# Optimization experiments

Measured on AMD Instinct MI355X. Metric: run time of the kernel, lower is better.

## Reference

```python
import jax, jax.numpy as jnp
import numpy as np

D_MODEL = 1024
HEAD_SIZE = 64
BLOCK_SIZE = 2048
B, T = 4, 2048


def setup_inputs() -> dict:
    key = jax.random.key(0)
    ks = jax.random.split(key, 7)
    s = 1.0 / np.sqrt(D_MODEL)
    x = jax.random.normal(ks[0], (B, T, D_MODEL), dtype=jnp.float32)
    Wq = jax.random.uniform(ks[1], (D_MODEL, HEAD_SIZE), jnp.float32, -s, s)
    bq = jax.random.uniform(ks[2], (HEAD_SIZE,), jnp.float32, -s, s)
    Wk = jax.random.uniform(ks[3], (D_MODEL, HEAD_SIZE), jnp.float32, -s, s)
    bk = jax.random.uniform(ks[4], (HEAD_SIZE,), jnp.float32, -s, s)
    Wv = jax.random.uniform(ks[5], (D_MODEL, HEAD_SIZE), jnp.float32, -s, s)
    return {"x": x, "Wq": Wq, "bq": bq, "Wk": Wk, "bk": bk, "Wv": Wv, "mask": 1}


def reference(x, Wq, bq, Wk, bk, Wv, mask):
    # x: [B, T, C]; single attention head, dropout is identity (eval/p=0)
    Tlen = x.shape[1]
    q = x @ Wq + bq              # [B, T, hs]
    k = x @ Wk + bk              # [B, T, hs]
    v = x @ Wv                   # [B, T, hs] (no bias)
    hs = k.shape[-1]
    # Faithful to source: weights = QK^T / hs**(-0.5)  ==  QK^T * sqrt(hs)
    w = jnp.einsum('btd,bsd->bts', q, k) * jnp.sqrt(jnp.asarray(hs, x.dtype))
    if mask:
        causal = jnp.tril(jnp.ones((Tlen, Tlen), dtype=bool))
        w = jnp.where(causal, w, jnp.asarray(-jnp.inf, w.dtype))
    w = jax.nn.softmax(w, axis=-1)
    out = jnp.einsum('bts,bsd->btd', w, v)  # [B, T, hs]
    return out
```

## Files before the change

### kernel.cpp

```cpp
#include <hip/hip_runtime.h>
#include <hip/hip_bf16.h>

#define D_MODEL 1024
#define HS 64
#define T_LEN 2048
#define JCH 512
#define NCH 4

typedef __attribute__((ext_vector_type(8))) short bf16x8;
typedef __attribute__((ext_vector_type(4))) float f32x4;

__device__ inline void split8(const float* v, int4& hi, int4& lo) {
    union { unsigned short u[8]; int4 v4; } uh, ul;
    #pragma unroll
    for (int i = 0; i < 8; ++i) {
        const unsigned int b = __float_as_uint(v[i]);
        const unsigned short h = (unsigned short)(b >> 16);
        const float r = v[i] - __uint_as_float((unsigned int)h << 16);
        uh.u[i] = h;
        ul.u[i] = (unsigned short)(__float_as_uint(r) >> 16);
    }
    hi = uh.v4; lo = ul.v4;
}

__device__ inline unsigned short f2bf_rne(float f) {
    const unsigned int b = __float_as_uint(f);
    return (unsigned short)((b + 0x7FFFu + ((b >> 16) & 1u)) >> 16);
}
__device__ inline float bf2f(unsigned short h) {
    return __uint_as_float((unsigned int)h << 16);
}

__global__ __launch_bounds__(256) void wprep_kernel(
    const float* __restrict__ Wq, const float* __restrict__ Wk,
    const float* __restrict__ Wv, short* __restrict__ Wh, short* __restrict__ Wl)
{
    __shared__ float tile[64][69];
    const int tid = threadIdx.x;
    const int kb = blockIdx.x & 15;
    const int m  = blockIdx.x >> 4;
    const float* W = (m == 0) ? Wq : (m == 1) ? Wk : Wv;
    #pragma unroll
    for (int it = 0; it < 4; ++it) {
        const int idx = tid + 256 * it;
        const int kr = idx >> 4, c4 = idx & 15;
        *(float4*)&tile[kr][4 * c4] =
            *(const float4*)(W + (size_t)(kb * 64 + kr) * HS + 4 * c4);
    }
    __syncthreads();
    #pragma unroll
    for (int it = 0; it < 2; ++it) {
        const int s = tid + 256 * it;
        const int n = s >> 3, kc = s & 7;
        float v[8];
        #pragma unroll
        for (int i = 0; i < 8; ++i) v[i] = tile[kc * 8 + i][n];
        int4 hi, lo;
        split8(v, hi, lo);
        const size_t off = (size_t)(m * 64 + n) * D_MODEL + kb * 64 + kc * 8;
        *(int4*)(Wh + off) = hi;
        *(int4*)(Wl + off) = lo;
    }
}

__global__ __launch_bounds__(256, 2) void qkv_kernel(
    const float* __restrict__ x,
    const short* __restrict__ Wh, const short* __restrict__ Wl,
    const float* __restrict__ bq, const float* __restrict__ bk,
    float* __restrict__ q, float* __restrict__ k, float* __restrict__ vt, int BT)
{
    __shared__ __align__(16) short Ah[2 * 520], Al[2 * 520];
    __shared__ __align__(16) short Bh[6 * 520], Bl[6 * 520];

    const int tid  = threadIdx.x;
    const int r0   = blockIdx.x * 32;
    const int nb   = blockIdx.y;
    const int wave = tid >> 6;
    const int lane = tid & 63;
    const int mt_w = wave >> 1;
    const int nt0  = (wave & 1) * 3;

    f32x4 acc[3];
    #pragma unroll
    for (int j = 0; j < 3; ++j) acc[j] = (f32x4)(0.f);

    const bool doA = (tid >= 128);
    const int  au  = tid & 127;
    const int  amt = au >> 6;
    const int  aln = au & 63;
    const float* axsrc =
        x + (size_t)(r0 + amt * 16 + (aln & 15)) * D_MODEL + (aln >> 4) * 8;

    const int b0nt = tid >> 6;
    const int b0ln = tid & 63;
    const size_t b0off =
        (size_t)(nb * 96 + b0nt * 16 + (b0ln & 15)) * D_MODEL + (b0ln >> 4) * 8;
    const int b1nt = 4 + (tid >> 6);
    const int b1ln = tid & 63;
    const size_t b1off =
        (size_t)(nb * 96 + b1nt * 16 + (b1ln & 15)) * D_MODEL + (b1ln >> 4) * 8;

    float4 a0v, a1v;
    int4 b0h, b0l, b1h, b1l;
    if (doA) {
        a0v = *(const float4*)(axsrc);
        a1v = *(const float4*)(axsrc + 4);
    }
    b0h = *(const int4*)(Wh + b0off);
    b0l = *(const int4*)(Wl + b0off);
    if (!doA) {
        b1h = *(const int4*)(Wh + b1off);
        b1l = *(const int4*)(Wl + b1off);
    }

    for (int k0 = 0; k0 < D_MODEL; k0 += 32) {
        __syncthreads();
        if (doA) {
            float xv[8];
            *(float4*)&xv[0] = a0v;
            *(float4*)&xv[4] = a1v;
            int4 hi, lo;
            split8(xv, hi, lo);
            *(int4*)&Ah[amt * 520 + aln * 8] = hi;
            *(int4*)&Al[amt * 520 + aln * 8] = lo;
        }
        *(int4*)&Bh[b0nt * 520 + b0ln * 8] = b0h;
        *(int4*)&Bl[b0nt * 520 + b0ln * 8] = b0l;
        if (!doA) {
            *(int4*)&Bh[b1nt * 520 + b1ln * 8] = b1h;
            *(int4*)&Bl[b1nt * 520 + b1ln * 8] = b1l;
        }
        __syncthreads();
        const int kn = k0 + 32;
        if (kn < D_MODEL) {
            if (doA) {
                a0v = *(const float4*)(axsrc + kn);
                a1v = *(const float4*)(axsrc + kn + 4);
            }
            b0h = *(const int4*)(Wh + b0off + kn);
            b0l = *(const int4*)(Wl + b0off + kn);
            if (!doA) {
                b1h = *(const int4*)(Wh + b1off + kn);
                b1l = *(const int4*)(Wl + b1off + kn);
            }
        }
        const bf16x8 afh = *(const bf16x8*)&Ah[mt_w * 520 + lane * 8];
        const bf16x8 afl = *(const bf16x8*)&Al[mt_w * 520 + lane * 8];
        #pragma unroll
        for (int j = 0; j < 3; ++j) {
            const int nt = nt0 + j;
            const bf16x8 bfh = *(const bf16x8*)&Bh[nt * 520 + lane * 8];
            const bf16x8 bfl = *(const bf16x8*)&Bl[nt * 520 + lane * 8];
            acc[j] = __builtin_amdgcn_mfma_f32_16x16x32_bf16(afh, bfh, acc[j], 0, 0, 0);
            acc[j] = __builtin_amdgcn_mfma_f32_16x16x32_bf16(afh, bfl, acc[j], 0, 0, 0);
            acc[j] = __builtin_amdgcn_mfma_f32_16x16x32_bf16(afl, bfh, acc[j], 0, 0, 0);
        }
    }

    const int rowb = r0 + mt_w * 16 + (lane >> 4) * 4;
    #pragma unroll
    for (int j = 0; j < 3; ++j) {
        const int c = nb * 96 + (nt0 + j) * 16 + (lane & 15);
        if (c < 64) {
            const float bias = bq[c];
            #pragma unroll
            for (int r = 0; r < 4; ++r)
                q[(size_t)(rowb + r) * HS + c] = acc[j][r] + bias;
        } else if (c < 128) {
            const float bias = bk[c - 64];
            #pragma unroll
            for (int r = 0; r < 4; ++r)
                k[(size_t)(rowb + r) * HS + (c - 64)] = acc[j][r] + bias;
        } else {
            float4 o;
            o.x = acc[j][0]; o.y = acc[j][1]; o.z = acc[j][2]; o.w = acc[j][3];
            *(float4*)(vt + (size_t)(c - 128) * BT + rowb) = o;
        }
    }
}

__global__ __launch_bounds__(256) void attn_kernel(
    const float* __restrict__ q_ws, const float* __restrict__ k_ws,
    const float* __restrict__ vt_ws, const int* __restrict__ maskp,
    float* __restrict__ part_O, float* __restrict__ part_ml, int BT)
{
    __shared__ __align__(16) short Kh[4096], Kl[4096];
    __shared__ __align__(16) short Vt[4096];
    __shared__ __align__(16) short Pl[4][16 * 72];

    const int tile  = blockIdx.x;
    const int chunk = blockIdx.y;
    const int r0 = tile * 64;
    const int tb = r0 / T_LEN;
    const int t0 = r0 - tb * T_LEN;
    const int mask = (*maskp != 0);
    const int n_max = mask ? (t0 + 64) : T_LEN;
    const int j0 = chunk * JCH;
    if (j0 >= n_max) return;
    const int hi_j = min(j0 + JCH, n_max);
    const int njt = (hi_j - j0 + 63) >> 6;

    const int tid  = threadIdx.x;
    const int w    = tid >> 6;
    const int lane = tid & 63;
    const int quad = lane >> 4;
    const int l15  = lane & 15;
    const int rw0  = t0 + 16 * w;
    const int rowa = r0 + 16 * w + quad * 4;

    bf16x8 qfh[2], qfl[2];
    {
        const float* qrow = q_ws + (size_t)(r0 + 16 * w + l15) * HS + quad * 8;
        #pragma unroll
        for (int kc = 0; kc < 2; ++kc) {
            float v[8];
            *(float4*)&v[0] = *(const float4*)(qrow + kc * 32);
            *(float4*)&v[4] = *(const float4*)(qrow + kc * 32 + 4);
            union { int4 i; bf16x8 b; } ch, cl;
            split8(v, ch.i, cl.i);
            qfh[kc] = ch.b;
            qfl[kc] = cl.b;
        }
    }

    f32x4 oacc[4];
    #pragma unroll
    for (int nt = 0; nt < 4; ++nt) oacc[nt] = (f32x4)(0.f);
    float m_r[4] = {-INFINITY, -INFINITY, -INFINITY, -INFINITY};
    float l_r[4] = {0.f, 0.f, 0.f, 0.f};

    const float* kbase = k_ws + (size_t)tb * T_LEN * HS;

    for (int jt = 0; jt < njt; ++jt) {
        const int jbase = j0 + jt * 64;
        __syncthreads();
        #pragma unroll
        for (int it = 0; it < 2; ++it) {
            const int s  = tid + 256 * it;
            const int ls = s & 63;
            const int sc = s >> 6;
            const int jsub = sc >> 1, kc = sc & 1;
            const int jrow = jbase + jsub * 16 + (ls & 15);
            const int koff = kc * 32 + (ls >> 4) * 8;
            const float* src = kbase + (size_t)jrow * HS + koff;
            float v[8];
            *(float4*)&v[0] = *(const float4*)src;
            *(float4*)&v[4] = *(const float4*)(src + 4);
            int4 hi, lo;
            split8(v, hi, lo);
            *(int4*)&Kh[s * 8] = hi;
            *(int4*)&Kl[s * 8] = lo;
        }
        #pragma unroll
        for (int it = 0; it < 2; ++it) {
            const int s  = tid + 256 * it;
            const int ls = s & 63;
            const int sc = s >> 6;
            const int jc = sc >> 2, nt = sc & 3;
            const int n  = nt * 16 + (ls & 15);
            const int jcol = jbase + jc * 32 + (ls >> 4) * 8;
            const float* src = vt_ws + (size_t)n * BT + tb * T_LEN + jcol;
            float v[8];
            *(float4*)&v[0] = *(const float4*)src;
            *(float4*)&v[4] = *(const float4*)(src + 4);
            union { unsigned short u[8]; int4 i; } pk;
            #pragma unroll
            for (int i = 0; i < 8; ++i) pk.u[i] = f2bf_rne(v[i]);
            *(int4*)&Vt[s * 8] = pk.i;
        }
        __syncthreads();

        const bool active = (!mask) || (jbase <= rw0 + 15);
        if (active) {
            f32x4 sacc[4];
            #pragma unroll
            for (int jsub = 0; jsub < 4; ++jsub) {
                f32x4 s = (f32x4)(0.f);
                #pragma unroll
                for (int kc = 0; kc < 2; ++kc) {
                    const bf16x8 kh = *(const bf16x8*)&Kh[((jsub * 2 + kc) * 64 + lane) * 8];
                    const bf16x8 kl = *(const bf16x8*)&Kl[((jsub * 2 + kc) * 64 + lane) * 8];
                    s = __builtin_amdgcn_mfma_f32_16x16x32_bf16(qfh[kc], kh, s, 0, 0, 0);
                    s = __builtin_amdgcn_mfma_f32_16x16x32_bf16(qfh[kc], kl, s, 0, 0, 0);
                    s = __builtin_amdgcn_mfma_f32_16x16x32_bf16(qfl[kc], kh, s, 0, 0, 0);
                }
                sacc[jsub] = s;
            }
            float sval[4][4], rmax[4];
            #pragma unroll
            for (int r = 0; r < 4; ++r) rmax[r] = -INFINITY;
            #pragma unroll
            for (int jsub = 0; jsub < 4; ++jsub) {
                const int jg = jbase + jsub * 16 + l15;
                #pragma unroll
                for (int r = 0; r < 4; ++r) {
                    const int tg = rw0 + quad * 4 + r;
                    const float vv = (mask && (jg > tg)) ? -INFINITY : 8.0f * sacc[jsub][r];
                    sval[jsub][r] = vv;
                    rmax[r] = fmaxf(rmax[r], vv);
                }
            }
            #pragma unroll
            for (int d = 1; d < 16; d <<= 1)
                #pragma unroll
                for (int r = 0; r < 4; ++r)
                    rmax[r] = fmaxf(rmax[r], __shfl_xor(rmax[r], d));
            float alpha[4], msafe[4];
            #pragma unroll
            for (int r = 0; r < 4; ++r) {
                const float mn = fmaxf(m_r[r], rmax[r]);
                msafe[r] = (mn == -INFINITY) ? 0.f : mn;
                alpha[r] = __expf(m_r[r] - msafe[r]);
                m_r[r] = mn;
            }
            short* Pw = &Pl[w][0];
            float rsum[4] = {0.f, 0.f, 0.f, 0.f};
            #pragma unroll
            for (int jsub = 0; jsub < 4; ++jsub) {
                #pragma unroll
                for (int r = 0; r < 4; ++r) {
                    const float e = __expf(sval[jsub][r] - msafe[r]);
                    const unsigned short eb = f2bf_rne(e);
                    Pw[(quad * 4 + r) * 72 + jsub * 16 + l15] = (short)eb;
                    rsum[r] += bf2f(eb);
                }
            }
            #pragma unroll
            for (int d = 1; d < 16; d <<= 1)
                #pragma unroll
                for (int r = 0; r < 4; ++r)
                    rsum[r] += __shfl_xor(rsum[r], d);
            #pragma unroll
            for (int r = 0; r < 4; ++r)
                l_r[r] = l_r[r] * alpha[r] + rsum[r];
            #pragma unroll
            for (int nt = 0; nt < 4; ++nt)
                #pragma unroll
                for (int r = 0; r < 4; ++r)
                    oacc[nt][r] *= alpha[r];
            bf16x8 pf[2];
            #pragma unroll
            for (int jc = 0; jc < 2; ++jc)
                pf[jc] = *(const bf16x8*)&Pw[l15 * 72 + jc * 32 + quad * 8];
            #pragma unroll
            for (int nt = 0; nt < 4; ++nt) {
                #pragma unroll
                for (int jc = 0; jc < 2; ++jc) {
                    const bf16x8 vf = *(const bf16x8*)&Vt[((jc * 4 + nt) * 64 + lane) * 8];
                    oacc[nt] = __builtin_amdgcn_mfma_f32_16x16x32_bf16(pf[jc], vf, oacc[nt], 0, 0, 0);
                }
            }
        }
    }

    #pragma unroll
    for (int nt = 0; nt < 4; ++nt)
        #pragma unroll
        for (int r = 0; r < 4; ++r)
            part_O[((size_t)(rowa + r) * NCH + chunk) * HS + nt * 16 + l15] = oacc[nt][r];
    if (l15 == 0) {
        #pragma unroll
        for (int r = 0; r < 4; ++r) {
            float2 ml;
            ml.x = m_r[r];
            ml.y = l_r[r];
            *(float2*)(part_ml + ((size_t)(rowa + r) * NCH + chunk) * 2) = ml;
        }
    }
}

__global__ __launch_bounds__(256) void combine_kernel(
    const float* __restrict__ part_O, const float* __restrict__ part_ml,
    const int* __restrict__ maskp, float* __restrict__ out)
{
    const int f = blockIdx.x * 256 + threadIdx.x;
    const int row = f >> 6;
    const int d = f & 63;
    const int t = row & (T_LEN - 1);
    const int mask = (*maskp != 0);
    const int n = mask ? (t + 1) : T_LEN;
    const int nc = (n + JCH - 1) / JCH;

    float mv[NCH], lv[NCH];
    float M = -INFINITY;
    for (int c = 0; c < nc; ++c) {
        const float2 ml = *(const float2*)(part_ml + ((size_t)row * NCH + c) * 2);
        mv[c] = ml.x; lv[c] = ml.y;
        M = fmaxf(M, ml.x);
    }
    float L = 0.f, O = 0.f;
    for (int c = 0; c < nc; ++c) {
        const float w = __expf(mv[c] - M);
        L += lv[c] * w;
        O = fmaf(part_O[((size_t)row * NCH + c) * HS + d], w, O);
    }
    out[(size_t)row * HS + d] = O / L;
}

extern "C" void kernel_launch(void* const* d_in, const int* in_sizes, int n_in,
                              void* d_out, int out_size, void* d_ws, size_t ws_size,
                              hipStream_t stream) {
    const float* x  = (const float*)d_in[0];
    const float* Wq = (const float*)d_in[1];
    const float* bq = (const float*)d_in[2];
    const float* Wk = (const float*)d_in[3];
    const float* bk = (const float*)d_in[4];
    const float* Wv = (const float*)d_in[5];
    const int* maskp = (const int*)d_in[6];

    const int BT = in_sizes[0] / D_MODEL;

    float* q   = (float*)d_ws;
    float* k   = q + (size_t)BT * HS;
    float* vt  = k + (size_t)BT * HS;
    float* pO  = vt + (size_t)BT * HS;
    float* pml = pO + (size_t)BT * NCH * HS;

    short* Wh = (short*)pO;
    short* Wl = Wh + (size_t)192 * D_MODEL;

    wprep_kernel<<<48, 256, 0, stream>>>(Wq, Wk, Wv, Wh, Wl);
    dim3 qgrid(BT / 32, 2);
    qkv_kernel<<<qgrid, 256, 0, stream>>>(x, Wh, Wl, bq, bk, q, k, vt, BT);
    dim3 agrid(BT / 64, NCH);
    attn_kernel<<<agrid, 256, 0, stream>>>(q, k, vt, maskp, pO, pml, BT);
    combine_kernel<<<(BT * HS) / 256, 256, 0, stream>>>(pO, pml, maskp, (float*)d_out);
}
```

Before: 156.0 us.

## Halve QKV and attention block sizes and prefetch next K/V tiles into registers

The QKV projection kernel now uses 128-thread blocks covering 16 rows instead of 32, so there are twice as many blocks. Each wave now loads several weight fragments. The attention kernel now uses 2-wave blocks over 32 query rows, which doubles the grid and makes the causal cutoff finer. It also software-prefetches the next K/V tile from global memory into registers while the current tile is computed. The costs are higher register pressure from the prefetch buffers and more redundant K/V loading, since each key tile is now read by twice as many blocks.

```diff
diff --git a/kernel.cpp b/kernel.cpp
--- a/kernel.cpp
+++ b/kernel.cpp
@@ -63,89 +63,84 @@
     }
 }
 
-__global__ __launch_bounds__(256, 2) void qkv_kernel(
+__global__ __launch_bounds__(128, 2) void qkv_kernel(
     const float* __restrict__ x,
     const short* __restrict__ Wh, const short* __restrict__ Wl,
     const float* __restrict__ bq, const float* __restrict__ bk,
     float* __restrict__ q, float* __restrict__ k, float* __restrict__ vt, int BT)
 {
-    __shared__ __align__(16) short Ah[2 * 520], Al[2 * 520];
+    __shared__ __align__(16) short Ah[520], Al[520];
     __shared__ __align__(16) short Bh[6 * 520], Bl[6 * 520];
 
     const int tid  = threadIdx.x;
-    const int r0   = blockIdx.x * 32;
+    const int r0   = blockIdx.x * 16;
     const int nb   = blockIdx.y;
     const int wave = tid >> 6;
     const int lane = tid & 63;
-    const int mt_w = wave >> 1;
-    const int nt0  = (wave & 1) * 3;
+    const int nt0  = wave * 3;
 
     f32x4 acc[3];
     #pragma unroll
     for (int j = 0; j < 3; ++j) acc[j] = (f32x4)(0.f);
 
-    const bool doA = (tid >= 128);
-    const int  au  = tid & 127;
-    const int  amt = au >> 6;
-    const int  aln = au & 63;
     const float* axsrc =
-        x + (size_t)(r0 + amt * 16 + (aln & 15)) * D_MODEL + (aln >> 4) * 8;
-
-    const int b0nt = tid >> 6;
-    const int b0ln = tid & 63;
-    const size_t b0off =
-        (size_t)(nb * 96 + b0nt * 16 + (b0ln & 15)) * D_MODEL + (b0ln >> 4) * 8;
-    const int b1nt = 4 + (tid >> 6);
-    const int b1ln = tid & 63;
-    const size_t b1off =
-        (size_t)(nb * 96 + b1nt * 16 + (b1ln & 15)) * D_MODEL + (b1ln >> 4) * 8;
+        x + (size_t)(r0 + (lane & 15)) * D_MODEL + (lane >> 4) * 8;
+
+    size_t boff[4];
+    const int nB = wave ? 4 : 2;
+    #pragma unroll
+    for (int i = 0; i < 4; ++i) {
+        const int ntb = wave ? (2 + i) : i;
+        boff[i] = (size_t)(nb * 96 + ntb * 16 + (lane & 15)) * D_MODEL + (lane >> 4) * 8;
+    }
 
     float4 a0v, a1v;
-    int4 b0h, b0l, b1h, b1l;
-    if (doA) {
+    int4 pbh[4], pbl[4];
+    if (wave == 0) {
         a0v = *(const float4*)(axsrc);
         a1v = *(const float4*)(axsrc + 4);
     }
-    b0h = *(const int4*)(Wh + b0off);
-    b0l = *(const int4*)(Wl + b0off);
-    if (!doA) {
-        b1h = *(const int4*)(Wh + b1off);
-        b1l = *(const int4*)(Wl + b1off);
-    }
+    #pragma unroll
+    for (int i = 0; i < 4; ++i)
+        if (i < nB) {
+            pbh[i] = *(const int4*)(Wh + boff[i]);
+            pbl[i] = *(const int4*)(Wl + boff[i]);
+        }
 
     for (int k0 = 0; k0 < D_MODEL; k0 += 32) {
         __syncthreads();
-        if (doA) {
+        if (wave == 0) {
             float xv[8];
             *(float4*)&xv[0] = a0v;
             *(float4*)&xv[4] = a1v;
             int4 hi, lo;
             split8(xv, hi, lo);
-            *(int4*)&Ah[amt * 520 + aln * 8] = hi;
-            *(int4*)&Al[amt * 520 + aln * 8] = lo;
-        }
-        *(int4*)&Bh[b0nt * 520 + b0ln * 8] = b0h;
-        *(int4*)&Bl[b0nt * 520 + b0ln * 8] = b0l;
-        if (!doA) {
-            *(int4*)&Bh[b1nt * 520 + b1ln * 8] = b1h;
-            *(int4*)&Bl[b1nt * 520 + b1ln * 8] = b1l;
-        }
+            *(int4*)&Ah[lane * 8] = hi;
+            *(int4*)&Al[lane * 8] = lo;
+        }
+        #pragma unroll
+        for (int i = 0; i < 4; ++i)
+            if (i < nB) {
+                const int ntb = wave ? (2 + i) : i;
+                *(int4*)&Bh[ntb * 520 + lane * 8] = pbh[i];
+                *(int4*)&Bl[ntb * 520 + lane * 8] = pbl[i];
+            }
         __syncthreads();
         const int kn = k0 + 32;
         if (kn < D_MODEL) {
-            if (doA) {
+            if (wave == 0) {
                 a0v = *(const float4*)(axsrc + kn);
                 a1v = *(const float4*)(axsrc + kn + 4);
             }
-            b0h = *(const int4*)(Wh + b0off + kn);
-            b0l = *(const int4*)(Wl + b0off + kn);
-            if (!doA) {
-                b1h = *(const int4*)(Wh + b1off + kn);
-                b1l = *(const int4*)(Wl + b1off + kn);
-            }
-        }
-        const bf16x8 afh = *(const bf16x8*)&Ah[mt_w * 520 + lane * 8];
-        const bf16x8 afl = *(const bf16x8*)&Al[mt_w * 520 + lane * 8];
+            #pragma unroll
+            for (int i = 0; i < 4; ++i)
+                if (i < nB) {
+                    pbh[i] = *(const int4*)(Wh + boff[i] + kn);
+                    pbl[i] = *(const int4*)(Wl + boff[i] + kn);
+                }
+        }
+        const bf16x8 afh = *(const bf16x8*)&Ah[lane * 8];
+        const bf16x8 afl = *(const bf16x8*)&Al[lane * 8];
         #pragma unroll
         for (int j = 0; j < 3; ++j) {
             const int nt = nt0 + j;
@@ -157,7 +152,7 @@
         }
     }
 
-    const int rowb = r0 + mt_w * 16 + (lane >> 4) * 4;
+    const int rowb = r0 + (lane >> 4) * 4;
     #pragma unroll
     for (int j = 0; j < 3; ++j) {
         const int c = nb * 96 + (nt0 + j) * 16 + (lane & 15);
@@ -179,22 +174,22 @@
     }
 }
 
-__global__ __launch_bounds__(256) void attn_kernel(
+__global__ __launch_bounds__(128) void attn_kernel(
     const float* __restrict__ q_ws, const float* __restrict__ k_ws,
     const float* __restrict__ vt_ws, const int* __restrict__ maskp,
     float* __restrict__ part_O, float* __restrict__ part_ml, int BT)
 {
     __shared__ __align__(16) short Kh[4096], Kl[4096];
     __shared__ __align__(16) short Vt[4096];
-    __shared__ __align__(16) short Pl[4][16 * 72];
+    __shared__ __align__(16) short Pl[2][16 * 72];
 
     const int tile  = blockIdx.x;
     const int chunk = blockIdx.y;
-    const int r0 = tile * 64;
+    const int r0 = tile * 32;
     const int tb = r0 / T_LEN;
     const int t0 = r0 - tb * T_LEN;
     const int mask = (*maskp != 0);
-    const int n_max = mask ? (t0 + 64) : T_LEN;
+    const int n_max = mask ? (t0 + 32) : T_LEN;
     const int j0 = chunk * JCH;
     if (j0 >= n_max) return;
     const int hi_j = min(j0 + JCH, n_max);
@@ -230,45 +225,61 @@
     float l_r[4] = {0.f, 0.f, 0.f, 0.f};
 
     const float* kbase = k_ws + (size_t)tb * T_LEN * HS;
+    const float* vbase = vt_ws + (size_t)tb * T_LEN;
+
+    float4 pKa[4], pKb[4], pVa[4], pVb[4];
+    auto load_tiles = [&](int jb) {
+        #pragma unroll
+        for (int it = 0; it < 4; ++it) {
+            const int s  = tid + 128 * it;
+            const int ls = s & 63;
+            const int sc = s >> 6;
+            {
+                const int jsub = sc >> 1, kc = sc & 1;
+                const float* src = kbase + (size_t)(jb + jsub * 16 + (ls & 15)) * HS
+                                         + kc * 32 + (ls >> 4) * 8;
+                pKa[it] = *(const float4*)src;
+                pKb[it] = *(const float4*)(src + 4);
+            }
+            {
+                const int jc = sc >> 2, nt = sc & 3;
+                const float* src = vbase + (size_t)(nt * 16 + (ls & 15)) * BT
+                                         + jb + jc * 32 + (ls >> 4) * 8;
+                pVa[it] = *(const float4*)src;
+                pVb[it] = *(const float4*)(src + 4);
+            }
+        }
+    };
+
+    load_tiles(j0);
 
     for (int jt = 0; jt < njt; ++jt) {
         const int jbase = j0 + jt * 64;
         __syncthreads();
         #pragma unroll
-        for (int it = 0; it < 2; ++it) {
-            const int s  = tid + 256 * it;
-            const int ls = s & 63;
-            const int sc = s >> 6;
-            const int jsub = sc >> 1, kc = sc & 1;
-            const int jrow = jbase + jsub * 16 + (ls & 15);
-            const int koff = kc * 32 + (ls >> 4) * 8;
-            const float* src = kbase + (size_t)jrow * HS + koff;
-            float v[8];
-            *(float4*)&v[0] = *(const float4*)src;
-            *(float4*)&v[4] = *(const float4*)(src + 4);
-            int4 hi, lo;
-            split8(v, hi, lo);
-            *(int4*)&Kh[s * 8] = hi;
-            *(int4*)&Kl[s * 8] = lo;
-        }
-        #pragma unroll
-        for (int it = 0; it < 2; ++it) {
-            const int s  = tid + 256 * it;
-            const int ls = s & 63;
-            const int sc = s >> 6;
-            const int jc = sc >> 2, nt = sc & 3;
-            const int n  = nt * 16 + (ls & 15);
-            const int jcol = jbase + jc * 32 + (ls >> 4) * 8;
-            const float* src = vt_ws + (size_t)n * BT + tb * T_LEN + jcol;
-            float v[8];
-            *(float4*)&v[0] = *(const float4*)src;
-            *(float4*)&v[4] = *(const float4*)(src + 4);
-            union { unsigned short u[8]; int4 i; } pk;
-            #pragma unroll
-            for (int i = 0; i < 8; ++i) pk.u[i] = f2bf_rne(v[i]);
-            *(int4*)&Vt[s * 8] = pk.i;
+        for (int it = 0; it < 4; ++it) {
+            const int s = tid + 128 * it;
+            {
+                float v[8];
+                *(float4*)&v[0] = pKa[it];
+                *(float4*)&v[4] = pKb[it];
+                int4 hi, lo;
+                split8(v, hi, lo);
+                *(int4*)&Kh[s * 8] = hi;
+                *(int4*)&Kl[s * 8] = lo;
+            }
+            {
+                float v[8];
+                *(float4*)&v[0] = pVa[it];
+                *(float4*)&v[4] = pVb[it];
+                union { unsigned short u[8]; int4 i; } pk;
+                #pragma unroll
+                for (int i = 0; i < 8; ++i) pk.u[i] = f2bf_rne(v[i]);
+                *(int4*)&Vt[s * 8] = pk.i;
+            }
         }
         __syncthreads();
+        load_tiles((jt + 1 < njt) ? (jbase + 64) : jbase);
 
         const bool active = (!mask) || (jbase <= rw0 + 15);
         if (active) {
@@ -420,9 +431,9 @@
     short* Wl = Wh + (size_t)192 * D_MODEL;
 
     wprep_kernel<<<48, 256, 0, stream>>>(Wq, Wk, Wv, Wh, Wl);
-    dim3 qgrid(BT / 32, 2);
-    qkv_kernel<<<qgrid, 256, 0, stream>>>(x, Wh, Wl, bq, bk, q, k, vt, BT);
-    dim3 agrid(BT / 64, NCH);
-    attn_kernel<<<agrid, 256, 0, stream>>>(q, k, vt, maskp, pO, pml, BT);
+    dim3 qgrid(BT / 16, 2);
+    qkv_kernel<<<qgrid, 128, 0, stream>>>(x, Wh, Wl, bq, bk, q, k, vt, BT);
+    dim3 agrid(BT / 32, NCH);
+    attn_kernel<<<agrid, 128, 0, stream>>>(q, k, vt, maskp, pO, pml, BT);
     combine_kernel<<<(BT * HS) / 256, 256, 0, stream>>>(pO, pml, maskp, (float*)d_out);
 }
```

Measured after the change: 250.3 us. 1.61x slower.

## Split QKV projection into three column groups and double-buffer register prefetch

Applied to the files above, without the earlier changes.

The QKV projection grid grows from two to three column blocks, so each block computes 64 output columns instead of 96. Each wave now holds two accumulators, and B-tile staging becomes uniform across all threads. Global loads are prefetched two k-steps ahead using ping-pong register buffers, which hides more memory latency. The cost is reading each x tile three times instead of twice, plus more registers for the prefetch buffers.

```diff
diff --git a/kernel.cpp b/kernel.cpp
--- a/kernel.cpp
+++ b/kernel.cpp
@@ -70,7 +70,7 @@
     float* __restrict__ q, float* __restrict__ k, float* __restrict__ vt, int BT)
 {
     __shared__ __align__(16) short Ah[2 * 520], Al[2 * 520];
-    __shared__ __align__(16) short Bh[6 * 520], Bl[6 * 520];
+    __shared__ __align__(16) short Bh[4 * 520], Bl[4 * 520];
 
     const int tid  = threadIdx.x;
     const int r0   = blockIdx.x * 32;
@@ -78,11 +78,11 @@
     const int wave = tid >> 6;
     const int lane = tid & 63;
     const int mt_w = wave >> 1;
-    const int nt0  = (wave & 1) * 3;
-
-    f32x4 acc[3];
-    #pragma unroll
-    for (int j = 0; j < 3; ++j) acc[j] = (f32x4)(0.f);
+    const int nt0  = (wave & 1) * 2;
+
+    f32x4 acc[2];
+    acc[0] = (f32x4)(0.f);
+    acc[1] = (f32x4)(0.f);
 
     const bool doA = (tid >= 128);
     const int  au  = tid & 127;
@@ -91,63 +91,52 @@
     const float* axsrc =
         x + (size_t)(r0 + amt * 16 + (aln & 15)) * D_MODEL + (aln >> 4) * 8;
 
-    const int b0nt = tid >> 6;
-    const int b0ln = tid & 63;
-    const size_t b0off =
-        (size_t)(nb * 96 + b0nt * 16 + (b0ln & 15)) * D_MODEL + (b0ln >> 4) * 8;
-    const int b1nt = 4 + (tid >> 6);
-    const int b1ln = tid & 63;
-    const size_t b1off =
-        (size_t)(nb * 96 + b1nt * 16 + (b1ln & 15)) * D_MODEL + (b1ln >> 4) * 8;
-
-    float4 a0v, a1v;
-    int4 b0h, b0l, b1h, b1l;
+    const int bnt = tid >> 6;
+    const int bln = tid & 63;
+    const size_t boff =
+        (size_t)(nb * 64 + bnt * 16 + (bln & 15)) * D_MODEL + (bln >> 4) * 8;
+
+    float4 a0[2], a1[2];
+    int4 pbh[2], pbl[2];
     if (doA) {
-        a0v = *(const float4*)(axsrc);
-        a1v = *(const float4*)(axsrc + 4);
-    }
-    b0h = *(const int4*)(Wh + b0off);
-    b0l = *(const int4*)(Wl + b0off);
-    if (!doA) {
-        b1h = *(const int4*)(Wh + b1off);
-        b1l = *(const int4*)(Wl + b1off);
-    }
+        a0[0] = *(const float4*)(axsrc);
+        a1[0] = *(const float4*)(axsrc + 4);
+        a0[1] = *(const float4*)(axsrc + 32);
+        a1[1] = *(const float4*)(axsrc + 36);
+    }
+    pbh[0] = *(const int4*)(Wh + boff);
+    pbl[0] = *(const int4*)(Wl + boff);
+    pbh[1] = *(const int4*)(Wh + boff + 32);
+    pbl[1] = *(const int4*)(Wl + boff + 32);
 
     for (int k0 = 0; k0 < D_MODEL; k0 += 32) {
+        const int p = (k0 >> 5) & 1;
         __syncthreads();
         if (doA) {
             float xv[8];
-            *(float4*)&xv[0] = a0v;
-            *(float4*)&xv[4] = a1v;
+            *(float4*)&xv[0] = a0[p];
+            *(float4*)&xv[4] = a1[p];
             int4 hi, lo;
             split8(xv, hi, lo);
             *(int4*)&Ah[amt * 520 + aln * 8] = hi;
             *(int4*)&Al[amt * 520 + aln * 8] = lo;
         }
-        *(int4*)&Bh[b0nt * 520 + b0ln * 8] = b0h;
-        *(int4*)&Bl[b0nt * 520 + b0ln * 8] = b0l;
-        if (!doA) {
-            *(int4*)&Bh[b1nt * 520 + b1ln * 8] = b1h;
-            *(int4*)&Bl[b1nt * 520 + b1ln * 8] = b1l;
-        }
+        *(int4*)&Bh[bnt * 520 + bln * 8] = pbh[p];
+        *(int4*)&Bl[bnt * 520 + bln * 8] = pbl[p];
         __syncthreads();
-        const int kn = k0 + 32;
+        const int kn = k0 + 64;
         if (kn < D_MODEL) {
             if (doA) {
-                a0v = *(const float4*)(axsrc + kn);
-                a1v = *(const float4*)(axsrc + kn + 4);
-            }
-            b0h = *(const int4*)(Wh + b0off + kn);
-            b0l = *(const int4*)(Wl + b0off + kn);
-            if (!doA) {
-                b1h = *(const int4*)(Wh + b1off + kn);
-                b1l = *(const int4*)(Wl + b1off + kn);
-            }
+                a0[p] = *(const float4*)(axsrc + kn);
+                a1[p] = *(const float4*)(axsrc + kn + 4);
+            }
+            pbh[p] = *(const int4*)(Wh + boff + kn);
+            pbl[p] = *(const int4*)(Wl + boff + kn);
         }
         const bf16x8 afh = *(const bf16x8*)&Ah[mt_w * 520 + lane * 8];
         const bf16x8 afl = *(const bf16x8*)&Al[mt_w * 520 + lane * 8];
         #pragma unroll
-        for (int j = 0; j < 3; ++j) {
+        for (int j = 0; j < 2; ++j) {
             const int nt = nt0 + j;
             const bf16x8 bfh = *(const bf16x8*)&Bh[nt * 520 + lane * 8];
             const bf16x8 bfl = *(const bf16x8*)&Bl[nt * 520 + lane * 8];
@@ -159,8 +148,8 @@
 
     const int rowb = r0 + mt_w * 16 + (lane >> 4) * 4;
     #pragma unroll
-    for (int j = 0; j < 3; ++j) {
-        const int c = nb * 96 + (nt0 + j) * 16 + (lane & 15);
+    for (int j = 0; j < 2; ++j) {
+        const int c = nb * 64 + (nt0 + j) * 16 + (lane & 15);
         if (c < 64) {
             const float bias = bq[c];
             #pragma unroll
@@ -420,7 +409,7 @@
     short* Wl = Wh + (size_t)192 * D_MODEL;
 
     wprep_kernel<<<48, 256, 0, stream>>>(Wq, Wk, Wv, Wh, Wl);
-    dim3 qgrid(BT / 32, 2);
+    dim3 qgrid(BT / 32, 3);
     qkv_kernel<<<qgrid, 256, 0, stream>>>(x, Wh, Wl, bq, bk, q, k, vt, BT);
     dim3 agrid(BT / 64, NCH);
     attn_kernel<<<agrid, 256, 0, stream>>>(q, k, vt, maskp, pO, pml, BT);
```

Result: slower. 195.3 us (+25.3%).
